# Kernel optimization log

Measured on AMD Instinct MI355X. Metric: run time of the kernel, lower is better.

## Reference

```python
import jax, jax.numpy as jnp
import numpy as np

B, C, T = 64, 128, 4096
KNOT = 4  # default knot=4 -> 6 spline knots
SIGMA = 0.2


def setup_inputs() -> dict:
    key = jax.random.key(0)
    k1, k2, k3 = jax.random.split(key, 3)
    x = jax.random.normal(k1, (B, C, T), dtype=jnp.float32)
    # yy ~ N(1.0, sigma) as in GenerateRandomCurves
    yy = 1.0 + SIGMA * jax.random.normal(k2, (B, KNOT + 2, C), dtype=jnp.float32)
    mask_rand = jax.random.uniform(k3, (B, 1, 1), dtype=jnp.float32)
    return {"x": x, "yy": yy, "mask_rand": mask_rand}


def _notaknot_matrix(n, h):
    # Moment (second-derivative) system for a not-a-knot cubic spline on a
    # uniform grid with spacing h (matches scipy.interpolate.CubicSpline default bc).
    A = np.zeros((n, n), dtype=np.float32)
    for i in range(1, n - 1):
        A[i, i - 1] = h / 6.0
        A[i, i] = 2.0 * h / 3.0
        A[i, i + 1] = h / 6.0
    # not-a-knot: third derivative continuous at x1 and x_{n-2}
    A[0, 0], A[0, 1], A[0, 2] = 1.0, -2.0, 1.0
    A[-1, -3], A[-1, -2], A[-1, -1] = 1.0, -2.0, 1.0
    return jnp.asarray(A)


def reference(x, yy, mask_rand):
    Bq, Cq, Tq = x.shape
    n = KNOT + 2
    h = (Tq - 1) / (KNOT + 1)  # uniform knot spacing; knots span [0, T-1]
    A = _notaknot_matrix(n, h)

    # Solve for spline moments M (second derivatives at knots), batched over (B, C).
    rhs_int = (yy[:, 2:, :] - 2.0 * yy[:, 1:-1, :] + yy[:, :-2, :]) / h  # (B, n-2, C)
    z = jnp.zeros((Bq, 1, Cq), yy.dtype)
    rhs = jnp.concatenate([z, rhs_int, z], axis=1)  # (B, n, C)
    M = jnp.linalg.solve(A, rhs)  # (B, n, C)

    # Evaluate the spline at t = 0..T-1 (vectorized over all batch/channel).
    tq = jnp.arange(Tq, dtype=x.dtype)
    idx = jnp.clip(jnp.floor(tq / h).astype(jnp.int32), 0, n - 2)  # (T,)
    xl = idx.astype(x.dtype) * h
    dxl = (tq - xl)[None, :, None]       # t - x_i
    dxr = (xl + h - tq)[None, :, None]   # x_{i+1} - t
    Mi, Mi1 = M[:, idx, :], M[:, idx + 1, :]      # (B, T, C)
    yi, yi1 = yy[:, idx, :], yy[:, idx + 1, :]    # (B, T, C)
    curve = ((Mi * dxr**3 + Mi1 * dxl**3) / (6.0 * h)
             + (yi / h - Mi * h / 6.0) * dxr
             + (yi1 / h - Mi1 * h / 6.0) * dxl)   # (B, T, C)

    # DistortTimesteps: cumulative sum, rescaled so the last step lands on T-1.
    tt = jnp.cumsum(curve, axis=1)
    tt = tt * (Tq - 1) / tt[:, -1:, :]  # (B, T, C)

    # Per-(batch, channel) linear interpolation back onto the regular grid.
    xp = tt.transpose(0, 2, 1).reshape(Bq * Cq, Tq)  # warped timestamps
    fp = x.reshape(Bq * Cq, Tq)                      # channel signals
    x_tw = jax.vmap(lambda a, b: jnp.interp(tq, a, b))(xp, fp)
    x_tw = x_tw.reshape(Bq, Cq, Tq)

    mask = mask_rand < 0.5  # (B,1,1): apply warp with probability p=0.5
    return jnp.where(mask, x_tw, x)
```

## Files before the change

### kernel.cpp

```cpp
#include <hip/hip_runtime.h>

#define BB 64
#define CC 128
#define TT 4096
#define NN 6
#define HH 819.0f
#define NTHR 512
#define EPT 8
#define NWAVE (NTHR / 64)

typedef float f4 __attribute__((ext_vector_type(4)));

__device__ __forceinline__ void nt_store4(float* p, f4 v) {
    __builtin_nontemporal_store(v, (f4*)p);
}

__device__ __forceinline__ int padi(int j) { return j + (j >> 5); }

__global__ __launch_bounds__(NTHR) void timewarp_kernel(
    const float* __restrict__ x,
    const float* __restrict__ yy,
    const float* __restrict__ mask_rand,
    float* __restrict__ out)
{
    const int row = blockIdx.x;
    const int b   = row / CC;
    const int c   = row % CC;
    const int tid = threadIdx.x;

    const float* xrow = x + (size_t)row * TT;
    float* orow       = out + (size_t)row * TT;

    if (!(mask_rand[b] < 0.5f)) {
        const f4* xi = (const f4*)xrow;
        nt_store4(orow + 4 * tid,          xi[tid]);
        nt_store4(orow + 4 * (tid + NTHR), xi[tid + NTHR]);
        return;
    }

    __shared__ float sh_res[TT + TT / 32];
    __shared__ float sh_xx[NTHR];
    __shared__ float sh_fx[NTHR];
    __shared__ float sh_wsum[NWAVE];

    const int t0 = tid * EPT;
    float fpv[EPT];
    {
        const f4 v0 = *(const f4*)(xrow + t0);
        const f4 v1 = *(const f4*)(xrow + t0 + 4);
        fpv[0] = v0.x; fpv[1] = v0.y; fpv[2] = v0.z; fpv[3] = v0.w;
        fpv[4] = v1.x; fpv[5] = v1.y; fpv[6] = v1.z; fpv[7] = v1.w;
    }
    sh_fx[tid] = fpv[0];

    float Mv[NN];
    float y[NN];
    {
        #pragma unroll
        for (int k = 0; k < NN; ++k)
            y[k] = yy[((size_t)b * NN + k) * CC + c];
        float Aug[NN][NN + 1];
        #pragma unroll
        for (int i = 0; i < NN; ++i)
            #pragma unroll
            for (int j = 0; j < NN + 1; ++j)
                Aug[i][j] = 0.0f;
        Aug[0][0] = 1.0f;  Aug[0][1] = -2.0f;  Aug[0][2] = 1.0f;
        Aug[5][3] = 1.0f;  Aug[5][4] = -2.0f;  Aug[5][5] = 1.0f;
        #pragma unroll
        for (int i = 1; i < NN - 1; ++i) {
            Aug[i][i - 1] = HH / 6.0f;
            Aug[i][i]     = 2.0f * HH / 3.0f;
            Aug[i][i + 1] = HH / 6.0f;
            Aug[i][NN]    = (y[i + 1] - 2.0f * y[i] + y[i - 1]) / HH;
        }
        #pragma unroll
        for (int k = 0; k < NN; ++k) {
            float inv = 1.0f / Aug[k][k];
            #pragma unroll
            for (int i = k + 1; i < NN; ++i) {
                float m = Aug[i][k] * inv;
                #pragma unroll
                for (int j = k; j < NN + 1; ++j)
                    Aug[i][j] -= m * Aug[k][j];
            }
        }
        #pragma unroll
        for (int i = NN - 1; i >= 0; --i) {
            float s = Aug[i][NN];
            #pragma unroll
            for (int j = i + 1; j < NN; ++j)
                s -= Aug[i][j] * Mv[j];
            Mv[i] = s / Aug[i][i];
        }
    }

    int idxA = t0 / 819;  if (idxA > 4) idxA = 4;
    int idxB = idxA + 1;  if (idxB > 4) idxB = 4;
    float MiA = Mv[0], Mi1A = Mv[1], yiA = y[0], yi1A = y[1];
    #pragma unroll
    for (int s = 1; s <= 4; ++s)
        if (idxA >= s) { MiA = Mv[s]; Mi1A = Mv[s + 1]; yiA = y[s]; yi1A = y[s + 1]; }
    float MiB = Mv[0], Mi1B = Mv[1], yiB = y[0], yi1B = y[1];
    #pragma unroll
    for (int s = 1; s <= 4; ++s)
        if (idxB >= s) { MiB = Mv[s]; Mi1B = Mv[s + 1]; yiB = y[s]; yi1B = y[s + 1]; }
    const float invh  = 1.0f / HH;
    const float inv6h = 1.0f / (6.0f * HH);
    const float aA = yiA;
    const float bA = (yi1A - yiA) * invh - MiA * (HH / 3.0f) - Mi1A * (HH / 6.0f);
    const float cA = MiA * 0.5f;
    const float dA = (Mi1A - MiA) * inv6h;
    const float aB = yiB;
    const float bB = (yi1B - yiB) * invh - MiB * (HH / 3.0f) - Mi1B * (HH / 6.0f);
    const float cB = MiB * 0.5f;
    const float dB = (Mi1B - MiB) * inv6h;
    const float xlA = (float)idxA * HH;
    const float xlB = (float)idxB * HH;
    const float tb  = (float)((idxA + 1) * 819);

    float loc[EPT];
    float running = 0.0f;
    #pragma unroll
    for (int k = 0; k < EPT; ++k) {
        float ft = (float)(t0 + k);
        bool inB = ft >= tb;
        float xl = inB ? xlB : xlA;
        float ca = inB ? aB : aA;
        float cb = inB ? bB : bA;
        float cc = inB ? cB : cA;
        float cd = inB ? dB : dA;
        float s  = ft - xl;
        running += fmaf(s, fmaf(s, fmaf(s, cd, cc), cb), ca);
        loc[k] = running;
    }

    const int lane = tid & 63, wid = tid >> 6;
    float ws = running;
    #pragma unroll
    for (int d = 1; d < 64; d <<= 1) {
        float v = __shfl_up(ws, d, 64);
        if (lane >= d) ws += v;
    }
    if (lane == 63) sh_wsum[wid] = ws;
    __syncthreads();
    float wo = 0.0f, total = 0.0f;
    #pragma unroll
    for (int w = 0; w < NWAVE; ++w) {
        float s = sh_wsum[w];
        total += s;
        if (w < wid) wo += s;
    }
    const float offs  = wo + (ws - running);
    const float scale = 4095.0f / total;

    float xpv[EPT + 1];
    #pragma unroll
    for (int k = 0; k < EPT; ++k)
        xpv[k] = (loc[k] + offs) * scale;
    sh_xx[tid] = xpv[0];
    __syncthreads();
    xpv[EPT]        = (tid < NTHR - 1) ? sh_xx[tid + 1] : 4095.0f;
    const float fpb = (tid < NTHR - 1) ? sh_fx[tid + 1] : fpv[EPT - 1];

    #pragma unroll
    for (int k = 0; k < EPT; ++k) {
        const int seg = t0 + k;
        if (seg < TT - 1) {
            float xa = xpv[k], xb = xpv[k + 1];
            float fa = fpv[k];
            float fb = (k < EPT - 1) ? fpv[k + 1] : fpb;
            float d  = xb - xa;
            float slope = (d > 0.0f) ? (fb - fa) * __builtin_amdgcn_rcpf(d) : 0.0f;
            float a0 = fmaf(-xa, slope, fa);
            int qlo = (int)ceilf(xa);  if (qlo < 0) qlo = 0;
            int qhi = (int)ceilf(xb);  if (qhi > TT) qhi = TT;
            for (int q = qlo; q < qhi; ++q)
                sh_res[padi(q)] = fmaf((float)q, slope, a0);
        }
    }
    if (tid == 0) {
        int q1 = (int)ceilf(xpv[0]);  if (q1 > TT) q1 = TT;
        for (int q = 0; q < q1; ++q) sh_res[padi(q)] = fpv[0];
    }
    if (tid == NTHR - 1) {
        int q0 = (int)ceilf(xpv[EPT - 1]);  if (q0 < 0) q0 = 0;
        for (int q = q0; q < TT; ++q) sh_res[padi(q)] = fpv[EPT - 1];
    }
    __syncthreads();

    #pragma unroll
    for (int kk = 0; kk < 2; ++kk) {
        int i4 = tid + NTHR * kk;
        int fb4 = 4 * i4;
        int p  = padi(fb4);
        f4 v;
        v.x = sh_res[p + 0];
        v.y = sh_res[p + 1];
        v.z = sh_res[p + 2];
        v.w = sh_res[p + 3];
        nt_store4(orow + fb4, v);
    }
}

extern "C" void kernel_launch(void* const* d_in, const int* in_sizes, int n_in,
                              void* d_out, int out_size, void* d_ws, size_t ws_size,
                              hipStream_t stream) {
    const float* x    = (const float*)d_in[0];
    const float* yy   = (const float*)d_in[1];
    const float* mask = (const float*)d_in[2];
    float* out = (float*)d_out;
    timewarp_kernel<<<dim3(BB * CC), dim3(NTHR), 0, stream>>>(x, yy, mask, out);
}
```

Baseline: 232.0 us.

## Precompute per-row spline coefficients in a separate kernel and load from table

Adds a small pre-kernel that solves the 6x6 spline system once per (batch, channel) row and writes five cubic-segment coefficient vectors to the workspace. The main kernel then loads its two needed coefficient sets instead of having all 512 threads redundantly solve the system. The neighbour x value is now read directly from global memory rather than exchanged through shared memory. The cost is an extra kernel launch plus a dependency on a workspace buffer; without enough workspace it falls back to the old inline solve.

```diff
diff --git a/kernel.cpp b/kernel.cpp
--- a/kernel.cpp
+++ b/kernel.cpp
@@ -8,6 +8,9 @@
 #define NTHR 512
 #define EPT 8
 #define NWAVE (NTHR / 64)
+#define NROW (BB * CC)
+#define NSPAN 5
+#define TABBYTES ((size_t)NROW * NSPAN * 16)
 
 typedef float f4 __attribute__((ext_vector_type(4)));
 
@@ -17,15 +20,79 @@
 
 __device__ __forceinline__ int padi(int j) { return j + (j >> 5); }
 
+__device__ __forceinline__ void spline_solve(const float* __restrict__ yy,
+                                             int b, int c, float* y, float* Mv)
+{
+    #pragma unroll
+    for (int k = 0; k < NN; ++k)
+        y[k] = yy[((size_t)b * NN + k) * CC + c];
+    float Aug[NN][NN + 1];
+    #pragma unroll
+    for (int i = 0; i < NN; ++i)
+        #pragma unroll
+        for (int j = 0; j < NN + 1; ++j)
+            Aug[i][j] = 0.0f;
+    Aug[0][0] = 1.0f;  Aug[0][1] = -2.0f;  Aug[0][2] = 1.0f;
+    Aug[5][3] = 1.0f;  Aug[5][4] = -2.0f;  Aug[5][5] = 1.0f;
+    #pragma unroll
+    for (int i = 1; i < NN - 1; ++i) {
+        Aug[i][i - 1] = HH / 6.0f;
+        Aug[i][i]     = 2.0f * HH / 3.0f;
+        Aug[i][i + 1] = HH / 6.0f;
+        Aug[i][NN]    = (y[i + 1] - 2.0f * y[i] + y[i - 1]) / HH;
+    }
+    #pragma unroll
+    for (int k = 0; k < NN; ++k) {
+        float inv = 1.0f / Aug[k][k];
+        #pragma unroll
+        for (int i = k + 1; i < NN; ++i) {
+            float m = Aug[i][k] * inv;
+            #pragma unroll
+            for (int j = k; j < NN + 1; ++j)
+                Aug[i][j] -= m * Aug[k][j];
+        }
+    }
+    #pragma unroll
+    for (int i = NN - 1; i >= 0; --i) {
+        float s = Aug[i][NN];
+        #pragma unroll
+        for (int j = i + 1; j < NN; ++j)
+            s -= Aug[i][j] * Mv[j];
+        Mv[i] = s / Aug[i][i];
+    }
+}
+
+__global__ __launch_bounds__(256) void spline_coef_kernel(
+    const float* __restrict__ yy, f4* __restrict__ tab)
+{
+    const int row = blockIdx.x * 256 + threadIdx.x;
+    const int b = row / CC;
+    const int c = row % CC;
+    float y[NN], Mv[NN];
+    spline_solve(yy, b, c, y, Mv);
+    const float invh  = 1.0f / HH;
+    const float inv6h = 1.0f / (6.0f * HH);
+    #pragma unroll
+    for (int s = 0; s < NSPAN; ++s) {
+        f4 cf;
+        cf.x = y[s];
+        cf.y = (y[s + 1] - y[s]) * invh - Mv[s] * (HH / 3.0f) - Mv[s + 1] * (HH / 6.0f);
+        cf.z = Mv[s] * 0.5f;
+        cf.w = (Mv[s + 1] - Mv[s]) * inv6h;
+        tab[row * NSPAN + s] = cf;
+    }
+}
+
+template <int TABLE>
 __global__ __launch_bounds__(NTHR) void timewarp_kernel(
     const float* __restrict__ x,
     const float* __restrict__ yy,
     const float* __restrict__ mask_rand,
+    const f4* __restrict__ tab,
     float* __restrict__ out)
 {
     const int row = blockIdx.x;
     const int b   = row / CC;
-    const int c   = row % CC;
     const int tid = threadIdx.x;
 
     const float* xrow = x + (size_t)row * TT;
@@ -40,81 +107,48 @@
 
     __shared__ float sh_res[TT + TT / 32];
     __shared__ float sh_xx[NTHR];
-    __shared__ float sh_fx[NTHR];
     __shared__ float sh_wsum[NWAVE];
 
     const int t0 = tid * EPT;
-    float fpv[EPT];
-    {
-        const f4 v0 = *(const f4*)(xrow + t0);
-        const f4 v1 = *(const f4*)(xrow + t0 + 4);
-        fpv[0] = v0.x; fpv[1] = v0.y; fpv[2] = v0.z; fpv[3] = v0.w;
-        fpv[4] = v1.x; fpv[5] = v1.y; fpv[6] = v1.z; fpv[7] = v1.w;
-    }
-    sh_fx[tid] = fpv[0];
-
-    float Mv[NN];
-    float y[NN];
-    {
-        #pragma unroll
-        for (int k = 0; k < NN; ++k)
-            y[k] = yy[((size_t)b * NN + k) * CC + c];
-        float Aug[NN][NN + 1];
-        #pragma unroll
-        for (int i = 0; i < NN; ++i)
-            #pragma unroll
-            for (int j = 0; j < NN + 1; ++j)
-                Aug[i][j] = 0.0f;
-        Aug[0][0] = 1.0f;  Aug[0][1] = -2.0f;  Aug[0][2] = 1.0f;
-        Aug[5][3] = 1.0f;  Aug[5][4] = -2.0f;  Aug[5][5] = 1.0f;
-        #pragma unroll
-        for (int i = 1; i < NN - 1; ++i) {
-            Aug[i][i - 1] = HH / 6.0f;
-            Aug[i][i]     = 2.0f * HH / 3.0f;
-            Aug[i][i + 1] = HH / 6.0f;
-            Aug[i][NN]    = (y[i + 1] - 2.0f * y[i] + y[i - 1]) / HH;
-        }
-        #pragma unroll
-        for (int k = 0; k < NN; ++k) {
-            float inv = 1.0f / Aug[k][k];
-            #pragma unroll
-            for (int i = k + 1; i < NN; ++i) {
-                float m = Aug[i][k] * inv;
-                #pragma unroll
-                for (int j = k; j < NN + 1; ++j)
-                    Aug[i][j] -= m * Aug[k][j];
-            }
-        }
-        #pragma unroll
-        for (int i = NN - 1; i >= 0; --i) {
-            float s = Aug[i][NN];
-            #pragma unroll
-            for (int j = i + 1; j < NN; ++j)
-                s -= Aug[i][j] * Mv[j];
-            Mv[i] = s / Aug[i][i];
-        }
-    }
-
     int idxA = t0 / 819;  if (idxA > 4) idxA = 4;
     int idxB = idxA + 1;  if (idxB > 4) idxB = 4;
-    float MiA = Mv[0], Mi1A = Mv[1], yiA = y[0], yi1A = y[1];
-    #pragma unroll
-    for (int s = 1; s <= 4; ++s)
-        if (idxA >= s) { MiA = Mv[s]; Mi1A = Mv[s + 1]; yiA = y[s]; yi1A = y[s + 1]; }
-    float MiB = Mv[0], Mi1B = Mv[1], yiB = y[0], yi1B = y[1];
-    #pragma unroll
-    for (int s = 1; s <= 4; ++s)
-        if (idxB >= s) { MiB = Mv[s]; Mi1B = Mv[s + 1]; yiB = y[s]; yi1B = y[s + 1]; }
-    const float invh  = 1.0f / HH;
-    const float inv6h = 1.0f / (6.0f * HH);
-    const float aA = yiA;
-    const float bA = (yi1A - yiA) * invh - MiA * (HH / 3.0f) - Mi1A * (HH / 6.0f);
-    const float cA = MiA * 0.5f;
-    const float dA = (Mi1A - MiA) * inv6h;
-    const float aB = yiB;
-    const float bB = (yi1B - yiB) * invh - MiB * (HH / 3.0f) - Mi1B * (HH / 6.0f);
-    const float cB = MiB * 0.5f;
-    const float dB = (Mi1B - MiB) * inv6h;
+
+    const f4 v0 = *(const f4*)(xrow + t0);
+    const f4 v1 = *(const f4*)(xrow + t0 + 4);
+    const float fpb = xrow[(t0 + EPT < TT) ? (t0 + EPT) : (TT - 1)];
+
+    f4 cfA, cfB;
+    if (TABLE) {
+        cfA = tab[row * NSPAN + idxA];
+        cfB = tab[row * NSPAN + idxB];
+    } else {
+        const int c = row % CC;
+        float y[NN], Mv[NN];
+        spline_solve(yy, b, c, y, Mv);
+        const float invh  = 1.0f / HH;
+        const float inv6h = 1.0f / (6.0f * HH);
+        float MiA = Mv[0], Mi1A = Mv[1], yiA = y[0], yi1A = y[1];
+        #pragma unroll
+        for (int s = 1; s <= 4; ++s)
+            if (idxA >= s) { MiA = Mv[s]; Mi1A = Mv[s + 1]; yiA = y[s]; yi1A = y[s + 1]; }
+        float MiB = Mv[0], Mi1B = Mv[1], yiB = y[0], yi1B = y[1];
+        #pragma unroll
+        for (int s = 1; s <= 4; ++s)
+            if (idxB >= s) { MiB = Mv[s]; Mi1B = Mv[s + 1]; yiB = y[s]; yi1B = y[s + 1]; }
+        cfA.x = yiA;
+        cfA.y = (yi1A - yiA) * invh - MiA * (HH / 3.0f) - Mi1A * (HH / 6.0f);
+        cfA.z = MiA * 0.5f;
+        cfA.w = (Mi1A - MiA) * inv6h;
+        cfB.x = yiB;
+        cfB.y = (yi1B - yiB) * invh - MiB * (HH / 3.0f) - Mi1B * (HH / 6.0f);
+        cfB.z = MiB * 0.5f;
+        cfB.w = (Mi1B - MiB) * inv6h;
+    }
+
+    float fpv[EPT];
+    fpv[0] = v0.x; fpv[1] = v0.y; fpv[2] = v0.z; fpv[3] = v0.w;
+    fpv[4] = v1.x; fpv[5] = v1.y; fpv[6] = v1.z; fpv[7] = v1.w;
+
     const float xlA = (float)idxA * HH;
     const float xlB = (float)idxB * HH;
     const float tb  = (float)((idxA + 1) * 819);
@@ -125,13 +159,10 @@
     for (int k = 0; k < EPT; ++k) {
         float ft = (float)(t0 + k);
         bool inB = ft >= tb;
+        f4    cf = inB ? cfB : cfA;
         float xl = inB ? xlB : xlA;
-        float ca = inB ? aB : aA;
-        float cb = inB ? bB : bA;
-        float cc = inB ? cB : cA;
-        float cd = inB ? dB : dA;
         float s  = ft - xl;
-        running += fmaf(s, fmaf(s, fmaf(s, cd, cc), cb), ca);
+        running += fmaf(s, fmaf(s, fmaf(s, cf.w, cf.z), cf.y), cf.x);
         loc[k] = running;
     }
 
@@ -160,8 +191,7 @@
         xpv[k] = (loc[k] + offs) * scale;
     sh_xx[tid] = xpv[0];
     __syncthreads();
-    xpv[EPT]        = (tid < NTHR - 1) ? sh_xx[tid + 1] : 4095.0f;
-    const float fpb = (tid < NTHR - 1) ? sh_fx[tid + 1] : fpv[EPT - 1];
+    xpv[EPT] = (tid < NTHR - 1) ? sh_xx[tid + 1] : 4095.0f;
 
     #pragma unroll
     for (int k = 0; k < EPT; ++k) {
@@ -210,5 +240,12 @@
     const float* yy   = (const float*)d_in[1];
     const float* mask = (const float*)d_in[2];
     float* out = (float*)d_out;
-    timewarp_kernel<<<dim3(BB * CC), dim3(NTHR), 0, stream>>>(x, yy, mask, out);
-}
+
+    if (d_ws != nullptr && ws_size >= TABBYTES) {
+        f4* tab = (f4*)d_ws;
+        spline_coef_kernel<<<dim3(NROW / 256), dim3(256), 0, stream>>>(yy, tab);
+        timewarp_kernel<1><<<dim3(NROW), dim3(NTHR), 0, stream>>>(x, yy, mask, tab, out);
+    } else {
+        timewarp_kernel<0><<<dim3(NROW), dim3(NTHR), 0, stream>>>(x, yy, mask, nullptr, out);
+    }
+}
```

Result: no change. 235.4 us (+1.5%).
